# Kernel tuning notes

Measured on AMD Instinct MI355X. Metric: run time of the kernel, lower is better.

The kernel has to match this reference:

```python
import jax, jax.numpy as jnp
import numpy as np

K_GRAPH = 8
NUM_HEADS = 4


def _forward(kpt_feature, kpt_3d, gw1, gb1, gw2, gb2, w_q, b_q, w_k, b_k, w_v, b_v, w_a, b_a, w_o, b_o):
    B, N, D = kpt_feature.shape
    k = K_GRAPH
    H = NUM_HEADS
    hd = D // H

    # pairwise euclidean distances (b, N, N) -- torch.cdist equivalent
    sq = jnp.sum(kpt_3d * kpt_3d, axis=-1)
    d2 = sq[:, :, None] + sq[:, None, :] - 2.0 * jnp.einsum('bnc,bmc->bnm', kpt_3d, kpt_3d)
    dist = jnp.sqrt(jnp.maximum(d2, 0.0))

    # kNN excluding self (self-distance 0 sorts first)
    knn_idx = jnp.argsort(dist, axis=2)[:, :, 1:k + 1]  # (B, N, k)

    gather = jax.vmap(lambda arr, idx: arr[idx])  # per-batch fancy gather
    knn_pos = gather(kpt_3d, knn_idx)             # (B, N, k, 3)

    # geometry features (7-dim per edge)
    neighbor_dists = jnp.take_along_axis(dist, knn_idx, axis=2)   # (B, N, k)
    mean_dist = neighbor_dists.mean(axis=2, keepdims=True)        # (B, N, 1)
    std_dist = jnp.std(neighbor_dists, axis=2, ddof=1, keepdims=True)  # unbiased, like torch.std
    centroid = knn_pos.mean(axis=2)                               # (B, N, 3)
    rel = kpt_3d - centroid                                       # (B, N, 3)
    centered = knn_pos - centroid[:, :, None, :]                  # (B, N, k, 3)
    cov = jnp.einsum('bnkc,bnkd->bncd', centered, centered) / k   # (B, N, 3, 3)
    eig = jnp.linalg.eigvalsh(cov)                                # ascending
    aniso = eig[..., -1] / (eig[..., 0] + 1e-8)                   # (B, N)

    bcast = lambda x: jnp.broadcast_to(x[:, :, None, :], (B, N, k, x.shape[-1]))
    geom = jnp.concatenate([
        neighbor_dists[..., None],
        bcast(mean_dist),
        bcast(std_dist),
        bcast(rel),
        bcast(aniso[..., None]),
    ], axis=-1)                                                   # (B, N, k, 7)

    geom_agg = geom.mean(axis=2)                                  # (B, N, 7)
    enc = jax.nn.relu(geom_agg @ gw1.T + gb1) @ gw2.T + gb2       # (B, N, D)

    # gather-based graph attention
    knn_feat = gather(kpt_feature, knn_idx)                       # (B, N, k, D)
    Q = (kpt_feature @ w_q.T + b_q).reshape(B, N, H, hd)
    Kt = (knn_feat @ w_k.T + b_k).reshape(B, N, k, H, hd)
    Vt = (knn_feat @ w_v.T + b_v).reshape(B, N, k, H, hd)

    scores = jnp.einsum('bnhd,bnkhd->bnkh', Q, Kt) / (hd ** 0.5)  # (B, N, k, H)
    bias = geom @ w_a.T + b_a                                     # (B, N, k, H)
    attn = jax.nn.softmax(scores + bias, axis=2)
    agg = jnp.einsum('bnkh,bnkhd->bnhd', attn, Vt).reshape(B, N, D)
    graph_feat = agg @ w_o.T + b_o
    return enc + graph_feat


def setup_inputs() -> dict:
    key = jax.random.key(0)
    ks = jax.random.split(key, 20)
    B, N, D = 16, 2048, 256
    H = NUM_HEADS
    s = 0.05
    return {
        'kpt_feature': jax.random.normal(ks[0], (B, N, D), jnp.float32),
        'kpt_3d': jax.random.normal(ks[1], (B, N, 3), jnp.float32),
        'gw1': jax.random.normal(ks[2], (64, 7), jnp.float32) * s,
        'gb1': jax.random.normal(ks[3], (64,), jnp.float32) * s,
        'gw2': jax.random.normal(ks[4], (D, 64), jnp.float32) * s,
        'gb2': jax.random.normal(ks[5], (D,), jnp.float32) * s,
        'w_q': jax.random.normal(ks[6], (D, D), jnp.float32) * s,
        'b_q': jax.random.normal(ks[7], (D,), jnp.float32) * s,
        'w_k': jax.random.normal(ks[8], (D, D), jnp.float32) * s,
        'b_k': jax.random.normal(ks[9], (D,), jnp.float32) * s,
        'w_v': jax.random.normal(ks[10], (D, D), jnp.float32) * s,
        'b_v': jax.random.normal(ks[11], (D,), jnp.float32) * s,
        'w_a': jax.random.normal(ks[12], (H, 7), jnp.float32) * s,
        'b_a': jax.random.normal(ks[13], (H,), jnp.float32) * s,
        'w_o': jax.random.normal(ks[14], (D, D), jnp.float32) * s,
        'b_o': jax.random.normal(ks[15], (D,), jnp.float32) * s,
    }


def reference(kpt_feature, kpt_3d, gw1, gb1, gw2, gb2, w_q, b_q, w_k, b_k, w_v, b_v, w_a, b_a, w_o, b_o):
    return _forward(kpt_feature, kpt_3d, gw1, gb1, gw2, gb2, w_q, b_q, w_k, b_k, w_v, b_v, w_a, b_a, w_o, b_o)
```

## Files before the change

### kernel.cpp

```cpp
#include <hip/hip_runtime.h>
#include <math.h>

#define NN 2048

using f32x4 = __attribute__((ext_vector_type(4))) float;
using u32x4 = __attribute__((ext_vector_type(4))) unsigned int;
using u32x2 = __attribute__((ext_vector_type(2))) unsigned int;

__device__ __forceinline__ unsigned short f2bf(float x){
    unsigned int u = __float_as_uint(x);
    return (unsigned short)((u + 0x7FFFu + ((u>>16)&1u)) >> 16);
}
__device__ __forceinline__ float bf2f(unsigned short u){
    return __uint_as_float(((unsigned int)u) << 16);
}

__device__ __forceinline__ void mfma16(f32x4& acc, const u32x4& a, const u32x4& b) {
    asm("v_mfma_f32_16x16x32_bf16 %0, %1, %2, %0" : "+v"(acc) : "v"(a), "v"(b));
}

__device__ inline void eig3_minmax(double a11, double a12, double a13,
                                   double a22, double a23, double a33,
                                   double& lmin, double& lmax) {
    double p1 = a12*a12 + a13*a13 + a23*a23;
    double q  = (a11 + a22 + a33) / 3.0;
    double d1 = a11 - q, d2 = a22 - q, d3 = a33 - q;
    double p2 = d1*d1 + d2*d2 + d3*d3 + 2.0*p1;
    if (p2 <= 1e-300) { lmin = q; lmax = q; return; }
    double pp  = sqrt(p2 / 6.0);
    double inv = 1.0 / pp;
    double b11 = d1*inv, b22 = d2*inv, b33 = d3*inv;
    double b12 = a12*inv, b13 = a13*inv, b23 = a23*inv;
    double detB = b11*(b22*b33 - b23*b23) - b12*(b12*b33 - b23*b13) + b13*(b12*b23 - b22*b13);
    double r = detB * 0.5;
    r = fmin(1.0, fmax(-1.0, r));
    double phi = acos(r) / 3.0;
    lmax = q + 2.0*pp*cos(phi);
    lmin = q + 2.0*pp*cos(phi + 2.0943951023931953);
}

__global__ __launch_bounds__(256) void pack_pos(const float* __restrict__ k3,
                                                float4* __restrict__ pk) {
    const int i = blockIdx.x * 256 + threadIdx.x;
    const float x = k3[i*3+0], y = k3[i*3+1], z = k3[i*3+2];
    pk[i] = make_float4(x, y, z, x*x + y*y + z*z);
}

__global__ __launch_bounds__(256) void conv_feat(const float* __restrict__ in,
                                                 unsigned short* __restrict__ outb) {
    const size_t i = (size_t)(blockIdx.x * 256 + threadIdx.x) * 8;
    const float4 a = *(const float4*)(in + i);
    const float4 b = *(const float4*)(in + i + 4);
    u32x4 v;
    v.x = (unsigned)f2bf(a.x) | ((unsigned)f2bf(a.y) << 16);
    v.y = (unsigned)f2bf(a.z) | ((unsigned)f2bf(a.w) << 16);
    v.z = (unsigned)f2bf(b.x) | ((unsigned)f2bf(b.y) << 16);
    v.w = (unsigned)f2bf(b.z) | ((unsigned)f2bf(b.w) << 16);
    *(u32x4*)(outb + i) = v;
}

__global__ __launch_bounds__(256) void conv_w(
    const float* __restrict__ w_q, const float* __restrict__ w_k,
    const float* __restrict__ w_v, const float* __restrict__ w_o,
    unsigned short* __restrict__ wb) {
    const int i = blockIdx.x * 256 + threadIdx.x;
    const int sel = i >> 13;
    const size_t off = (size_t)(i & 8191) * 8;
    const float* src = (sel == 0) ? w_q : (sel == 1) ? w_k : (sel == 2) ? w_v : w_o;
    const float4 a = *(const float4*)(src + off);
    const float4 b = *(const float4*)(src + off + 4);
    u32x4 v;
    v.x = (unsigned)f2bf(a.x) | ((unsigned)f2bf(a.y) << 16);
    v.y = (unsigned)f2bf(a.z) | ((unsigned)f2bf(a.w) << 16);
    v.z = (unsigned)f2bf(b.x) | ((unsigned)f2bf(b.y) << 16);
    v.w = (unsigned)f2bf(b.z) | ((unsigned)f2bf(b.w) << 16);
    *(u32x4*)(wb + (size_t)sel * 65536 + off) = v;
}

__global__ __launch_bounds__(256) void knn_kernel(const float4* __restrict__ pk4,
                                                  int* __restrict__ idxOut) {
    __shared__ unsigned long long hitbuf[4][16];
    __shared__ int hitcnt[4];
    const int wave = threadIdx.x >> 6, lane = threadIdx.x & 63;
    const int p = blockIdx.x * 4 + wave;
    const int b = p >> 11, n = p & (NN - 1);
    const float4* pb = pk4 + (size_t)b * NN;
    const float4 me = pb[n];
    const float xn2 = -2.f*me.x, yn2 = -2.f*me.y, zn2 = -2.f*me.z, cn = me.w;

    if (lane == 0) hitcnt[wave] = 0;

    float dk[8];
    #pragma unroll
    for (int t = 0; t < 8; ++t) dk[t] = 1e30f;
    float d2s[32];

    #define INS(c4, jj, s) { \
        float d2 = cn + c4.w; \
        d2 = fmaf(xn2, c4.x, d2); \
        d2 = fmaf(yn2, c4.y, d2); \
        d2 = fmaf(zn2, c4.z, d2); \
        if ((jj) == n) d2 = 1e30f; \
        d2s[s] = d2; \
        dk[7] = __builtin_amdgcn_fmed3f(dk[6], dk[7], d2); \
        dk[6] = __builtin_amdgcn_fmed3f(dk[5], dk[6], d2); \
        dk[5] = __builtin_amdgcn_fmed3f(dk[4], dk[5], d2); \
        dk[4] = __builtin_amdgcn_fmed3f(dk[3], dk[4], d2); \
        dk[3] = __builtin_amdgcn_fmed3f(dk[2], dk[3], d2); \
        dk[2] = __builtin_amdgcn_fmed3f(dk[1], dk[2], d2); \
        dk[1] = __builtin_amdgcn_fmed3f(dk[0], dk[1], d2); \
        dk[0] = fminf(dk[0], d2); }

    #pragma unroll
    for (int i = 0; i < 8; ++i) {
        const int j0 = lane + i * 256;
        const float4 q0 = pb[j0];
        const float4 q1 = pb[j0 + 64];
        const float4 q2 = pb[j0 + 128];
        const float4 q3 = pb[j0 + 192];
        INS(q0, j0,       i*4 + 0)
        INS(q1, j0 + 64,  i*4 + 1)
        INS(q2, j0 + 128, i*4 + 2)
        INS(q3, j0 + 192, i*4 + 3)
    }
    #undef INS

    #define CSWAPV(a,c) { float lo = fminf(dk[a], dk[c]); float hi = fmaxf(dk[a], dk[c]); dk[a] = lo; dk[c] = hi; }
    #pragma unroll
    for (int m = 1; m < 64; m <<= 1) {
        float od[8];
        #pragma unroll
        for (int t = 0; t < 8; ++t) od[t] = __shfl_xor(dk[7 - t], m);
        #pragma unroll
        for (int t = 0; t < 8; ++t) dk[t] = fminf(dk[t], od[t]);
        CSWAPV(0,4) CSWAPV(1,5) CSWAPV(2,6) CSWAPV(3,7)
        CSWAPV(0,2) CSWAPV(1,3) CSWAPV(4,6) CSWAPV(5,7)
        CSWAPV(0,1) CSWAPV(2,3) CSWAPV(4,5) CSWAPV(6,7)
    }
    #undef CSWAPV

    const float tau = dk[7];

    #pragma unroll
    for (int s = 0; s < 32; ++s) {
        if (d2s[s] <= tau) {
            const int j = lane + (s >> 2) * 256 + (s & 3) * 64;
            unsigned u = __float_as_uint(d2s[s]);
            u ^= (u >> 31) ? 0xFFFFFFFFu : 0x80000000u;
            const int slot = atomicAdd(&hitcnt[wave], 1);
            if (slot < 16)
                hitbuf[wave][slot] = ((unsigned long long)u << 32) | (unsigned)j;
        }
    }

    if (lane == 0) {
        int cnt = hitcnt[wave]; if (cnt > 16) cnt = 16;
        int outv[8];
        if (cnt == 8) {
            #pragma unroll
            for (int t = 0; t < 8; ++t)
                outv[t] = (int)(unsigned)hitbuf[wave][t];
        } else {
            unsigned used = 0;
            #pragma unroll
            for (int t = 0; t < 8; ++t) {
                unsigned long long best = ~0ull; int bi = 0;
                #pragma unroll
                for (int i = 0; i < 16; ++i) {
                    unsigned long long v = (i < cnt && !((used >> i) & 1u))
                                         ? hitbuf[wave][i] : ~0ull;
                    if (v < best) { best = v; bi = i; }
                }
                used |= 1u << bi;
                outv[t] = (int)(unsigned)best;
            }
        }
        u32x4 v0; v0.x = outv[0]; v0.y = outv[1]; v0.z = outv[2]; v0.w = outv[3];
        u32x4 v1; v1.x = outv[4]; v1.y = outv[5]; v1.z = outv[6]; v1.w = outv[7];
        *(u32x4*)(idxOut + (size_t)p * 8)     = v0;
        *(u32x4*)(idxOut + (size_t)p * 8 + 4) = v1;
    }
}

__global__ __launch_bounds__(256) void geom_kernel(
    const float4* __restrict__ pk4, const int* __restrict__ knnIdx,
    const float* __restrict__ gw1, const float* __restrict__ gb1,
    const float* __restrict__ w_a, const float* __restrict__ b_a,
    float* __restrict__ biasOut, float* __restrict__ h32) {
    const int p = blockIdx.x * 256 + threadIdx.x;
    const int b = p >> 11, n = p & (NN - 1);
    const float4* pb = pk4 + (size_t)b * NN;
    const float4 me = pb[n];
    const float xn2 = -2.f*me.x, yn2 = -2.f*me.y, zn2 = -2.f*me.z, cn = me.w;

    int ik[8];
    *(u32x4*)&ik[0] = *(const u32x4*)(knnIdx + (size_t)p * 8);
    *(u32x4*)&ik[4] = *(const u32x4*)(knnIdx + (size_t)p * 8 + 4);

    float dist[8], px[8], py[8], pz[8];
    #pragma unroll
    for (int t = 0; t < 8; ++t) {
        const float4 q = pb[ik[t]];
        float d2 = cn + q.w;
        d2 = fmaf(xn2, q.x, d2);
        d2 = fmaf(yn2, q.y, d2);
        d2 = fmaf(zn2, q.z, d2);
        dist[t] = sqrtf(fmaxf(d2, 0.0f));
        px[t] = q.x; py[t] = q.y; pz[t] = q.z;
    }
    float mean = 0.f;
    #pragma unroll
    for (int t = 0; t < 8; ++t) mean += dist[t];
    mean *= 0.125f;
// ... 23 lines not shown
    float wa[28], ba[4];
    #pragma unroll
    for (int i = 0; i < 28; ++i) wa[i] = w_a[i];
    #pragma unroll
    for (int h = 0; h < 4; ++h) ba[h] = b_a[h];
    #pragma unroll
    for (int t = 0; t < 8; ++t) {
        f32x4 v;
        #pragma unroll
        for (int h = 0; h < 4; ++h) {
            v[h] = wa[h*7+0]*dist[t] + wa[h*7+1]*mean + wa[h*7+2]*stdd
                 + wa[h*7+3]*relx + wa[h*7+4]*rely + wa[h*7+5]*relz
                 + wa[h*7+6]*aniso + ba[h];
        }
        *(f32x4*)(biasOut + ((size_t)p*8 + t) * 4) = v;
    }

    const float g0 = mean, g1 = mean, g2 = stdd, g3 = relx, g4 = rely, g5 = relz, g6 = aniso;
    float* hrow = h32 + (size_t)p * 64;
    #pragma unroll
    for (int cq = 0; cq < 16; ++cq) {
        f32x4 hv;
        #pragma unroll
        for (int r = 0; r < 4; ++r) {
            const int c = cq*4 + r;
            float h = gw1[c*7+0]*g0 + gw1[c*7+1]*g1 + gw1[c*7+2]*g2 + gw1[c*7+3]*g3
                    + gw1[c*7+4]*g4 + gw1[c*7+5]*g5 + gw1[c*7+6]*g6 + gb1[c];
            hv[r] = fmaxf(h, 0.0f);
        }
        *(f32x4*)(hrow + cq*4) = hv;
    }
}

__global__ __launch_bounds__(256) void gemm_qkv_mfma(
    const unsigned short* __restrict__ Ab, const unsigned short* __restrict__ Wball,
    const float* __restrict__ b_q, const float* __restrict__ b_k, const float* __restrict__ b_v,
    float* __restrict__ Qb, unsigned short* __restrict__ Kb, unsigned short* __restrict__ Vb)
{
    __shared__ unsigned short As[128 * 72];
    __shared__ unsigned short Bs[128 * 72];
    const int tid = threadIdx.x;
    const int m0 = blockIdx.x * 128;
    const int wsel = blockIdx.y >> 1;
    const int crel0 = (blockIdx.y & 1) * 128;
    const unsigned short* Wb = Wball + (size_t)wsel * 65536;
    const float* bv = (wsel == 0) ? b_q : ((wsel == 1) ? b_k : b_v);

    const int sr = tid >> 1, sh = (tid & 1) * 32;
    const int wid = tid >> 6, lane = tid & 63;
    const int wr = (wid >> 1) * 64, wc = (wid & 1) * 64;
    const int l15 = lane & 15, lk = (lane >> 4) * 8, lq = (lane >> 4) * 4;

    f32x4 acc[4][4];
    #pragma unroll
    for (int i = 0; i < 4; ++i)
        #pragma unroll
        for (int j = 0; j < 4; ++j) { f32x4 z = {0.f,0.f,0.f,0.f}; acc[i][j] = z; }

    for (int k0 = 0; k0 < 256; k0 += 64) {
        const unsigned short* ga = Ab + (size_t)(m0 + sr) * 256 + k0 + sh;
        u32x4 a0 = *(const u32x4*)(ga);
        u32x4 a1 = *(const u32x4*)(ga + 8);
        u32x4 a2 = *(const u32x4*)(ga + 16);
        u32x4 a3 = *(const u32x4*)(ga + 24);
        const unsigned short* gw = Wb + (size_t)(crel0 + sr) * 256 + k0 + sh;
        u32x4 b0 = *(const u32x4*)(gw);
        u32x4 b1 = *(const u32x4*)(gw + 8);
        u32x4 b2 = *(const u32x4*)(gw + 16);
        u32x4 b3 = *(const u32x4*)(gw + 24);
        __syncthreads();
        *(u32x4*)&As[sr*72 + sh     ] = a0;
        *(u32x4*)&As[sr*72 + sh +  8] = a1;
        *(u32x4*)&As[sr*72 + sh + 16] = a2;
        *(u32x4*)&As[sr*72 + sh + 24] = a3;
        *(u32x4*)&Bs[sr*72 + sh     ] = b0;
        *(u32x4*)&Bs[sr*72 + sh +  8] = b1;
        *(u32x4*)&Bs[sr*72 + sh + 16] = b2;
        *(u32x4*)&Bs[sr*72 + sh + 24] = b3;
        __syncthreads();
        #pragma unroll
        for (int ks = 0; ks < 64; ks += 32) {
            u32x4 af[4], bfr[4];
            #pragma unroll
            for (int i = 0; i < 4; ++i)  af[i]  = *(const u32x4*)&As[(wr + i*16 + l15)*72 + ks + lk];
            #pragma unroll
            for (int j = 0; j < 4; ++j)  bfr[j] = *(const u32x4*)&Bs[(wc + j*16 + l15)*72 + ks + lk];
            #pragma unroll
            for (int i = 0; i < 4; ++i)
                #pragma unroll
                for (int j = 0; j < 4; ++j) mfma16(acc[i][j], af[i], bfr[j]);
        }
    }
    #pragma unroll
    for (int j = 0; j < 4; ++j) {
        const int col = crel0 + wc + j*16 + l15;
        const float biasv = bv[col];
        #pragma unroll
        for (int i = 0; i < 4; ++i)
            #pragma unroll
            for (int r = 0; r < 4; ++r) {
                const int m = m0 + wr + i*16 + lq + r;
                const float v = acc[i][j][r] + biasv;
                if (wsel == 0)      Qb[(size_t)m * 256 + col] = v;
                else if (wsel == 1) Kb[(size_t)m * 256 + col] = f2bf(v);
                else                Vb[(size_t)m * 256 + col] = f2bf(v);
            }
    }
}

__global__ __launch_bounds__(256) void gemm_o_mfma(
    const unsigned short* __restrict__ Ab, const unsigned short* __restrict__ Wb,
    const float* __restrict__ bvec, const float* addin, float* C)
{
    __shared__ unsigned short As[128 * 72];
    __shared__ unsigned short Bs[128 * 72];
    const int tid = threadIdx.x;
    const int m0 = blockIdx.x * 128;
    const int crel0 = blockIdx.y * 128;

    const int sr = tid >> 1, sh = (tid & 1) * 32;
    const int wid = tid >> 6, lane = tid & 63;
    const int wr = (wid >> 1) * 64, wc = (wid & 1) * 64;
    const int l15 = lane & 15, lk = (lane >> 4) * 8, lq = (lane >> 4) * 4;

    f32x4 acc[4][4];
    #pragma unroll
    for (int i = 0; i < 4; ++i)
        #pragma unroll
        for (int j = 0; j < 4; ++j) { f32x4 z = {0.f,0.f,0.f,0.f}; acc[i][j] = z; }

    for (int k0 = 0; k0 < 256; k0 += 64) {
        const unsigned short* ga = Ab + (size_t)(m0 + sr) * 256 + k0 + sh;
        u32x4 a0 = *(const u32x4*)(ga);
        u32x4 a1 = *(const u32x4*)(ga + 8);
        u32x4 a2 = *(const u32x4*)(ga + 16);
        u32x4 a3 = *(const u32x4*)(ga + 24);
        const unsigned short* gw = Wb + (size_t)(crel0 + sr) * 256 + k0 + sh;
        u32x4 b0 = *(const u32x4*)(gw);
        u32x4 b1 = *(const u32x4*)(gw + 8);
        u32x4 b2 = *(const u32x4*)(gw + 16);
        u32x4 b3 = *(const u32x4*)(gw + 24);
        __syncthreads();
        *(u32x4*)&As[sr*72 + sh     ] = a0;
        *(u32x4*)&As[sr*72 + sh +  8] = a1;
        *(u32x4*)&As[sr*72 + sh + 16] = a2;
        *(u32x4*)&As[sr*72 + sh + 24] = a3;
        *(u32x4*)&Bs[sr*72 + sh     ] = b0;
        *(u32x4*)&Bs[sr*72 + sh +  8] = b1;
        *(u32x4*)&Bs[sr*72 + sh + 16] = b2;
        *(u32x4*)&Bs[sr*72 + sh + 24] = b3;
        __syncthreads();
        #pragma unroll
        for (int ks = 0; ks < 64; ks += 32) {
            u32x4 af[4], bfr[4];
            #pragma unroll
            for (int i = 0; i < 4; ++i)  af[i]  = *(const u32x4*)&As[(wr + i*16 + l15)*72 + ks + lk];
            #pragma unroll
            for (int j = 0; j < 4; ++j)  bfr[j] = *(const u32x4*)&Bs[(wc + j*16 + l15)*72 + ks + lk];
            #pragma unroll
            for (int i = 0; i < 4; ++i)
                #pragma unroll
                for (int j = 0; j < 4; ++j) mfma16(acc[i][j], af[i], bfr[j]);
        }
    }
    #pragma unroll
    for (int j = 0; j < 4; ++j) {
        const int col = crel0 + wc + j*16 + l15;
        const float biasv = bvec[col];
        #pragma unroll
        for (int i = 0; i < 4; ++i)
            #pragma unroll
            for (int r = 0; r < 4; ++r) {
                const int m = m0 + wr + i*16 + lq + r;
                const float ad = addin[(size_t)m * 256 + col];
                C[(size_t)m * 256 + col] = acc[i][j][r] + biasv + ad;
            }
    }
}

template<int K>
__global__ __launch_bounds__(256) void gemm_f32_big(
    const float* __restrict__ A, const float* __restrict__ W,
    const float* __restrict__ bvec, float* __restrict__ C)
{
    __shared__ float As[16][132];
    __shared__ float Bs[16][132];
    const int tid = threadIdx.x;
    const int m0 = blockIdx.x * 128;
    const int c0 = blockIdx.y * 128;
    const int tx = tid & 15;
    const int ty = tid >> 4;
    const int lr = tid & 127;
    const int kh = (tid >> 7) * 8;

    float acc[8][8] = {};

    const float* ga = A + (size_t)(m0 + lr) * K + kh;
    const float* gb = W + (size_t)(c0 + lr) * K + kh;

    float4 av0 = *(const float4*)(ga);
    float4 av1 = *(const float4*)(ga + 4);
    float4 bv0 = *(const float4*)(gb);
    float4 bv1 = *(const float4*)(gb + 4);

    for (int k0 = 0; k0 < K; k0 += 16) {
        __syncthreads();
        As[kh+0][lr]=av0.x; As[kh+1][lr]=av0.y; As[kh+2][lr]=av0.z; As[kh+3][lr]=av0.w;
        As[kh+4][lr]=av1.x; As[kh+5][lr]=av1.y; As[kh+6][lr]=av1.z; As[kh+7][lr]=av1.w;
        Bs[kh+0][lr]=bv0.x; Bs[kh+1][lr]=bv0.y; Bs[kh+2][lr]=bv0.z; Bs[kh+3][lr]=bv0.w;
        Bs[kh+4][lr]=bv1.x; Bs[kh+5][lr]=bv1.y; Bs[kh+6][lr]=bv1.z; Bs[kh+7][lr]=bv1.w;
        if (k0 + 16 < K) {
            av0 = *(const float4*)(ga + k0 + 16);
            av1 = *(const float4*)(ga + k0 + 20);
            bv0 = *(const float4*)(gb + k0 + 16);
            bv1 = *(const float4*)(gb + k0 + 20);
        }
        __syncthreads();
        #pragma unroll
        for (int kk = 0; kk < 16; ++kk) {
            const float4 a0 = *(const float4*)&As[kk][ty*8];
            const float4 a1 = *(const float4*)&As[kk][ty*8+4];
            const float4 b0 = *(const float4*)&Bs[kk][tx*8];
            const float4 b1 = *(const float4*)&Bs[kk][tx*8+4];
            const float a[8] = {a0.x,a0.y,a0.z,a0.w,a1.x,a1.y,a1.z,a1.w};
            const float b[8] = {b0.x,b0.y,b0.z,b0.w,b1.x,b1.y,b1.z,b1.w};
            #pragma unroll
            for (int i = 0; i < 8; ++i)
                #pragma unroll
                for (int j = 0; j < 8; ++j)
                    acc[i][j] = fmaf(a[i], b[j], acc[i][j]);
        }
    }
    #pragma unroll
    for (int i = 0; i < 8; ++i) {
        const size_t m = m0 + ty*8 + i;
        const int c = c0 + tx*8;
        float4 v0, v1;
        v0.x = acc[i][0] + bvec[c+0];
        v0.y = acc[i][1] + bvec[c+1];
        v0.z = acc[i][2] + bvec[c+2];
        v0.w = acc[i][3] + bvec[c+3];
        v1.x = acc[i][4] + bvec[c+4];
        v1.y = acc[i][5] + bvec[c+5];
        v1.z = acc[i][6] + bvec[c+6];
        v1.w = acc[i][7] + bvec[c+7];
        *(float4*)(C + m*256 + c)     = v0;
        *(float4*)(C + m*256 + c + 4) = v1;
    }
}

__global__ __launch_bounds__(256) void attn_kernel(
    const float* __restrict__ Qb, const unsigned short* __restrict__ Kb,
    const unsigned short* __restrict__ Vb, const int* __restrict__ knnIdx,
    const float* __restrict__ biasb, unsigned short* __restrict__ aggb)
{
    const int wave = threadIdx.x >> 6;
    const int lane = threadIdx.x & 63;
    const int B = blockIdx.x;
    const int xcd = B & 7;
    const int k = B >> 3;
    const int batch = xcd + ((k >= 512) ? 8 : 0);
    const int p = batch * NN + ((k & 511) << 2) + wave;
    const int b = batch;
    const int h = lane >> 4;

    const float4 q = *(const float4*)(Qb + (size_t)p*256 + lane*4);

    int g[8];
    #pragma unroll
    for (int t = 0; t < 8; ++t) g[t] = b * NN + knnIdx[(size_t)p*8 + t];

    float s[8];
    #pragma unroll
    for (int t = 0; t < 8; ++t) {
        const ushort4 kv = *(const ushort4*)(Kb + (size_t)g[t]*256 + lane*4);
        float acc = q.x * bf2f(kv.x);
        acc = fmaf(q.y, bf2f(kv.y), acc);
        acc = fmaf(q.z, bf2f(kv.z), acc);
        acc = fmaf(q.w, bf2f(kv.w), acc);
        acc += __shfl_xor(acc, 1);
        acc += __shfl_xor(acc, 2);
        acc += __shfl_xor(acc, 4);
        acc += __shfl_xor(acc, 8);
        s[t] = acc * 0.125f + biasb[((size_t)p*8 + t)*4 + h];
    }

    float mx = s[0];
    #pragma unroll
    for (int t = 1; t < 8; ++t) mx = fmaxf(mx, s[t]);
    float sum = 0.f;
    #pragma unroll
    for (int t = 0; t < 8; ++t) { s[t] = expf(s[t] - mx); sum += s[t]; }
    const float inv = 1.0f / sum;

    f32x4 a = {0.f, 0.f, 0.f, 0.f};
    #pragma unroll
    for (int t = 0; t < 8; ++t) {
        const float wgt = s[t] * inv;
        const ushort4 vv = *(const ushort4*)(Vb + (size_t)g[t]*256 + lane*4);
        a[0] = fmaf(wgt, bf2f(vv.x), a[0]);
        a[1] = fmaf(wgt, bf2f(vv.y), a[1]);
        a[2] = fmaf(wgt, bf2f(vv.z), a[2]);
        a[3] = fmaf(wgt, bf2f(vv.w), a[3]);
    }
    u32x2 pk;
    pk.x = (unsigned)f2bf(a[0]) | ((unsigned)f2bf(a[1]) << 16);
    pk.y = (unsigned)f2bf(a[2]) | ((unsigned)f2bf(a[3]) << 16);
    *(u32x2*)(aggb + (size_t)p*256 + lane*4) = pk;
}

extern "C" void kernel_launch(void* const* d_in, const int* in_sizes, int n_in,
                              void* d_out, int out_size, void* d_ws, size_t ws_size,
                              hipStream_t stream) {
    const float* feat = (const float*)d_in[0];
    const float* k3   = (const float*)d_in[1];
    const float* gw1  = (const float*)d_in[2];
    const float* gb1  = (const float*)d_in[3];
    const float* gw2  = (const float*)d_in[4];
    const float* gb2  = (const float*)d_in[5];
    const float* w_q  = (const float*)d_in[6];
    const float* b_q  = (const float*)d_in[7];
    const float* w_k  = (const float*)d_in[8];
    const float* b_k  = (const float*)d_in[9];
    const float* w_v  = (const float*)d_in[10];
    const float* b_v  = (const float*)d_in[11];
    const float* w_a  = (const float*)d_in[12];
    const float* b_a  = (const float*)d_in[13];
    const float* w_o  = (const float*)d_in[14];
    const float* b_o  = (const float*)d_in[15];
    float* out = (float*)d_out;

    char* w = (char*)d_ws;
    int*            knnIdx = (int*)w;
    float*          biasb  = (float*)(w + (size_t)1*(1u<<20));
    float*          Qb     = (float*)(w + (size_t)5*(1u<<20));
    unsigned short* Kb     = (unsigned short*)(w + (size_t)37*(1u<<20));
    unsigned short* Vb     = (unsigned short*)(w + (size_t)53*(1u<<20));
    float*          h32    = (float*)(w + (size_t)69*(1u<<20));
    float4*         pk4    = (float4*)(w + (size_t)78*(1u<<20));
    unsigned short* featb  = (unsigned short*)(w + (size_t)79*(1u<<20));
    unsigned short* wb     = (unsigned short*)(w + (size_t)95*(1u<<20));
    unsigned short* aggb   = featb;

    pack_pos<<<128, 256, 0, stream>>>(k3, pk4);
    conv_feat<<<4096, 256, 0, stream>>>(feat, featb);
    conv_w<<<128, 256, 0, stream>>>(w_q, w_k, w_v, w_o, wb);
    knn_kernel<<<8192, 256, 0, stream>>>(pk4, knnIdx);
    geom_kernel<<<128, 256, 0, stream>>>(pk4, knnIdx, gw1, gb1, w_a, b_a, biasb, h32);
    gemm_f32_big<64><<<dim3(256, 2), 256, 0, stream>>>(h32, gw2, gb2, out);
    gemm_qkv_mfma<<<dim3(256, 6), 256, 0, stream>>>(featb, wb, b_q, b_k, b_v, Qb, Kb, Vb);
    attn_kernel<<<8192, 256, 0, stream>>>(Qb, Kb, Vb, knnIdx, biasb, aggb);
    gemm_o_mfma<<<dim3(256, 2), 256, 0, stream>>>(aggb, wb + (size_t)3*65536, b_o, out, out);
}
```

Measured before the change: 181.9 us.

## Merge independent kernels into block-range-dispatched fused launches

Folds the three prep kernels into one launch. kNN and the QKV GEMM, which are independent, now run in one launch whose block index selects the task, and the geometry-encoder GEMM and attention are merged the same way. This cuts launch count from nine to five and lets independent work run concurrently on the GPU to fill idle compute units. In exchange, the fused kernels carry the larger shared-memory footprint of the GEMM branch, which may lower occupancy for the kNN and attention blocks.

```diff
diff --git a/kernel.cpp b/kernel.cpp
--- a/kernel.cpp
+++ b/kernel.cpp
@@ -39,146 +39,228 @@
     lmin = q + 2.0*pp*cos(phi + 2.0943951023931953);
 }
 
-__global__ __launch_bounds__(256) void pack_pos(const float* __restrict__ k3,
-                                                float4* __restrict__ pk) {
-    const int i = blockIdx.x * 256 + threadIdx.x;
-    const float x = k3[i*3+0], y = k3[i*3+1], z = k3[i*3+2];
-    pk[i] = make_float4(x, y, z, x*x + y*y + z*z);
-}
-
-__global__ __launch_bounds__(256) void conv_feat(const float* __restrict__ in,
-                                                 unsigned short* __restrict__ outb) {
-    const size_t i = (size_t)(blockIdx.x * 256 + threadIdx.x) * 8;
-    const float4 a = *(const float4*)(in + i);
-    const float4 b = *(const float4*)(in + i + 4);
-    u32x4 v;
-    v.x = (unsigned)f2bf(a.x) | ((unsigned)f2bf(a.y) << 16);
-    v.y = (unsigned)f2bf(a.z) | ((unsigned)f2bf(a.w) << 16);
-    v.z = (unsigned)f2bf(b.x) | ((unsigned)f2bf(b.y) << 16);
-    v.w = (unsigned)f2bf(b.z) | ((unsigned)f2bf(b.w) << 16);
-    *(u32x4*)(outb + i) = v;
-}
-
-__global__ __launch_bounds__(256) void conv_w(
+__global__ __launch_bounds__(256) void prep_kernel(
+    const float* __restrict__ k3, float4* __restrict__ pk,
+    const float* __restrict__ feat, unsigned short* __restrict__ featb,
     const float* __restrict__ w_q, const float* __restrict__ w_k,
     const float* __restrict__ w_v, const float* __restrict__ w_o,
-    unsigned short* __restrict__ wb) {
-    const int i = blockIdx.x * 256 + threadIdx.x;
-    const int sel = i >> 13;
-    const size_t off = (size_t)(i & 8191) * 8;
-    const float* src = (sel == 0) ? w_q : (sel == 1) ? w_k : (sel == 2) ? w_v : w_o;
-    const float4 a = *(const float4*)(src + off);
-    const float4 b = *(const float4*)(src + off + 4);
-    u32x4 v;
-    v.x = (unsigned)f2bf(a.x) | ((unsigned)f2bf(a.y) << 16);
-    v.y = (unsigned)f2bf(a.z) | ((unsigned)f2bf(a.w) << 16);
-    v.z = (unsigned)f2bf(b.x) | ((unsigned)f2bf(b.y) << 16);
-    v.w = (unsigned)f2bf(b.z) | ((unsigned)f2bf(b.w) << 16);
-    *(u32x4*)(wb + (size_t)sel * 65536 + off) = v;
-}
-
-__global__ __launch_bounds__(256) void knn_kernel(const float4* __restrict__ pk4,
-                                                  int* __restrict__ idxOut) {
+    unsigned short* __restrict__ wb)
+{
+    const int B = blockIdx.x;
+    if (B < 128) {
+        const int i = B * 256 + threadIdx.x;
+        const float x = k3[i*3+0], y = k3[i*3+1], z = k3[i*3+2];
+        pk[i] = make_float4(x, y, z, x*x + y*y + z*z);
+    } else if (B < 4224) {
+        const size_t i = (size_t)((B - 128) * 256 + threadIdx.x) * 8;
+        const float4 a = *(const float4*)(feat + i);
+        const float4 b = *(const float4*)(feat + i + 4);
+        u32x4 v;
+        v.x = (unsigned)f2bf(a.x) | ((unsigned)f2bf(a.y) << 16);
+        v.y = (unsigned)f2bf(a.z) | ((unsigned)f2bf(a.w) << 16);
+        v.z = (unsigned)f2bf(b.x) | ((unsigned)f2bf(b.y) << 16);
+        v.w = (unsigned)f2bf(b.z) | ((unsigned)f2bf(b.w) << 16);
+        *(u32x4*)(featb + i) = v;
+    } else {
+        const int i = (B - 4224) * 256 + threadIdx.x;
+        const int sel = i >> 13;
+        const size_t off = (size_t)(i & 8191) * 8;
+        const float* src = (sel == 0) ? w_q : (sel == 1) ? w_k : (sel == 2) ? w_v : w_o;
+        const float4 a = *(const float4*)(src + off);
+        const float4 b = *(const float4*)(src + off + 4);
+        u32x4 v;
+        v.x = (unsigned)f2bf(a.x) | ((unsigned)f2bf(a.y) << 16);
+        v.y = (unsigned)f2bf(a.z) | ((unsigned)f2bf(a.w) << 16);
+        v.z = (unsigned)f2bf(b.x) | ((unsigned)f2bf(b.y) << 16);
+        v.w = (unsigned)f2bf(b.z) | ((unsigned)f2bf(b.w) << 16);
+        *(u32x4*)(wb + (size_t)sel * 65536 + off) = v;
+    }
+}
+
+__global__ __launch_bounds__(256) void fused_knn_qkv(
+    const float4* __restrict__ pk4, int* __restrict__ idxOut,
+    const unsigned short* __restrict__ Ab, const unsigned short* __restrict__ Wball,
+    const float* __restrict__ b_q, const float* __restrict__ b_k, const float* __restrict__ b_v,
+    float* __restrict__ Qb, unsigned short* __restrict__ Kb, unsigned short* __restrict__ Vb)
+{
+    __shared__ unsigned short As[128 * 72];
+    __shared__ unsigned short Bs[128 * 72];
     __shared__ unsigned long long hitbuf[4][16];
     __shared__ int hitcnt[4];
-    const int wave = threadIdx.x >> 6, lane = threadIdx.x & 63;
-    const int p = blockIdx.x * 4 + wave;
-    const int b = p >> 11, n = p & (NN - 1);
-    const float4* pb = pk4 + (size_t)b * NN;
-    const float4 me = pb[n];
-    const float xn2 = -2.f*me.x, yn2 = -2.f*me.y, zn2 = -2.f*me.z, cn = me.w;
-
-    if (lane == 0) hitcnt[wave] = 0;
-
-    float dk[8];
-    #pragma unroll
-    for (int t = 0; t < 8; ++t) dk[t] = 1e30f;
-    float d2s[32];
-
-    #define INS(c4, jj, s) { \
-        float d2 = cn + c4.w; \
-        d2 = fmaf(xn2, c4.x, d2); \
-        d2 = fmaf(yn2, c4.y, d2); \
-        d2 = fmaf(zn2, c4.z, d2); \
-        if ((jj) == n) d2 = 1e30f; \
-        d2s[s] = d2; \
-        dk[7] = __builtin_amdgcn_fmed3f(dk[6], dk[7], d2); \
-        dk[6] = __builtin_amdgcn_fmed3f(dk[5], dk[6], d2); \
-        dk[5] = __builtin_amdgcn_fmed3f(dk[4], dk[5], d2); \
-        dk[4] = __builtin_amdgcn_fmed3f(dk[3], dk[4], d2); \
-        dk[3] = __builtin_amdgcn_fmed3f(dk[2], dk[3], d2); \
-        dk[2] = __builtin_amdgcn_fmed3f(dk[1], dk[2], d2); \
-        dk[1] = __builtin_amdgcn_fmed3f(dk[0], dk[1], d2); \
-        dk[0] = fminf(dk[0], d2); }
-
-    #pragma unroll
-    for (int i = 0; i < 8; ++i) {
-        const int j0 = lane + i * 256;
-        const float4 q0 = pb[j0];
-        const float4 q1 = pb[j0 + 64];
-        const float4 q2 = pb[j0 + 128];
-        const float4 q3 = pb[j0 + 192];
-        INS(q0, j0,       i*4 + 0)
-        INS(q1, j0 + 64,  i*4 + 1)
-        INS(q2, j0 + 128, i*4 + 2)
-        INS(q3, j0 + 192, i*4 + 3)
-    }
-    #undef INS
-
-    #define CSWAPV(a,c) { float lo = fminf(dk[a], dk[c]); float hi = fmaxf(dk[a], dk[c]); dk[a] = lo; dk[c] = hi; }
-    #pragma unroll
-    for (int m = 1; m < 64; m <<= 1) {
-        float od[8];
-        #pragma unroll
-        for (int t = 0; t < 8; ++t) od[t] = __shfl_xor(dk[7 - t], m);
-        #pragma unroll
-        for (int t = 0; t < 8; ++t) dk[t] = fminf(dk[t], od[t]);
-        CSWAPV(0,4) CSWAPV(1,5) CSWAPV(2,6) CSWAPV(3,7)
-        CSWAPV(0,2) CSWAPV(1,3) CSWAPV(4,6) CSWAPV(5,7)
-        CSWAPV(0,1) CSWAPV(2,3) CSWAPV(4,5) CSWAPV(6,7)
-    }
-    #undef CSWAPV
-
-    const float tau = dk[7];
-
-    #pragma unroll
-    for (int s = 0; s < 32; ++s) {
-        if (d2s[s] <= tau) {
-            const int j = lane + (s >> 2) * 256 + (s & 3) * 64;
-            unsigned u = __float_as_uint(d2s[s]);
-            u ^= (u >> 31) ? 0xFFFFFFFFu : 0x80000000u;
-            const int slot = atomicAdd(&hitcnt[wave], 1);
-            if (slot < 16)
-                hitbuf[wave][slot] = ((unsigned long long)u << 32) | (unsigned)j;
-        }
-    }
-
-    if (lane == 0) {
-        int cnt = hitcnt[wave]; if (cnt > 16) cnt = 16;
-        int outv[8];
-        if (cnt == 8) {
-            #pragma unroll
-            for (int t = 0; t < 8; ++t)
-                outv[t] = (int)(unsigned)hitbuf[wave][t];
-        } else {
-            unsigned used = 0;
-            #pragma unroll
-            for (int t = 0; t < 8; ++t) {
-                unsigned long long best = ~0ull; int bi = 0;
-                #pragma unroll
-                for (int i = 0; i < 16; ++i) {
-                    unsigned long long v = (i < cnt && !((used >> i) & 1u))
-                                         ? hitbuf[wave][i] : ~0ull;
-                    if (v < best) { best = v; bi = i; }
+
+    const int B = blockIdx.x;
+    const int tid = threadIdx.x;
+
+    if (B < 1536) {
+        const int idx = B;
+        const int by = idx % 6;
+        const int m0 = (idx / 6) * 128;
+        const int wsel = by >> 1;
+        const int crel0 = (by & 1) * 128;
+        const unsigned short* Wb = Wball + (size_t)wsel * 65536;
+        const float* bv = (wsel == 0) ? b_q : ((wsel == 1) ? b_k : b_v);
+
+        const int sr = tid >> 1, sh = (tid & 1) * 32;
+        const int wid = tid >> 6, lane = tid & 63;
+        const int wr = (wid >> 1) * 64, wc = (wid & 1) * 64;
+        const int l15 = lane & 15, lk = (lane >> 4) * 8, lq = (lane >> 4) * 4;
+
+        f32x4 acc[4][4];
+        #pragma unroll
+        for (int i = 0; i < 4; ++i)
+            #pragma unroll
+            for (int j = 0; j < 4; ++j) { f32x4 z = {0.f,0.f,0.f,0.f}; acc[i][j] = z; }
+
+        for (int k0 = 0; k0 < 256; k0 += 64) {
+            const unsigned short* ga = Ab + (size_t)(m0 + sr) * 256 + k0 + sh;
+            u32x4 a0 = *(const u32x4*)(ga);
+            u32x4 a1 = *(const u32x4*)(ga + 8);
+            u32x4 a2 = *(const u32x4*)(ga + 16);
+            u32x4 a3 = *(const u32x4*)(ga + 24);
+            const unsigned short* gw = Wb + (size_t)(crel0 + sr) * 256 + k0 + sh;
+            u32x4 b0 = *(const u32x4*)(gw);
+            u32x4 b1 = *(const u32x4*)(gw + 8);
+            u32x4 b2 = *(const u32x4*)(gw + 16);
+            u32x4 b3 = *(const u32x4*)(gw + 24);
+            __syncthreads();
+            *(u32x4*)&As[sr*72 + sh     ] = a0;
+            *(u32x4*)&As[sr*72 + sh +  8] = a1;
+            *(u32x4*)&As[sr*72 + sh + 16] = a2;
+            *(u32x4*)&As[sr*72 + sh + 24] = a3;
+            *(u32x4*)&Bs[sr*72 + sh     ] = b0;
+            *(u32x4*)&Bs[sr*72 + sh +  8] = b1;
+            *(u32x4*)&Bs[sr*72 + sh + 16] = b2;
+            *(u32x4*)&Bs[sr*72 + sh + 24] = b3;
+            __syncthreads();
+            #pragma unroll
+            for (int ks = 0; ks < 64; ks += 32) {
+                u32x4 af[4], bfr[4];
+                #pragma unroll
+                for (int i = 0; i < 4; ++i)  af[i]  = *(const u32x4*)&As[(wr + i*16 + l15)*72 + ks + lk];
+                #pragma unroll
+                for (int j = 0; j < 4; ++j)  bfr[j] = *(const u32x4*)&Bs[(wc + j*16 + l15)*72 + ks + lk];
+                #pragma unroll
+                for (int i = 0; i < 4; ++i)
+                    #pragma unroll
+                    for (int j = 0; j < 4; ++j) mfma16(acc[i][j], af[i], bfr[j]);
+            }
+        }
+        #pragma unroll
+        for (int j = 0; j < 4; ++j) {
+            const int col = crel0 + wc + j*16 + l15;
+            const float biasv = bv[col];
+            #pragma unroll
+            for (int i = 0; i < 4; ++i)
+                #pragma unroll
+                for (int r = 0; r < 4; ++r) {
+                    const int m = m0 + wr + i*16 + lq + r;
+                    const float v = acc[i][j][r] + biasv;
+                    if (wsel == 0)      Qb[(size_t)m * 256 + col] = v;
+                    else if (wsel == 1) Kb[(size_t)m * 256 + col] = f2bf(v);
+                    else                Vb[(size_t)m * 256 + col] = f2bf(v);
                 }
-                used |= 1u << bi;
-                outv[t] = (int)(unsigned)best;
+        }
+    } else {
+        const int blk = B - 1536;
+        const int wave = tid >> 6, lane = tid & 63;
+        const int p = blk * 4 + wave;
+        const int b = p >> 11, n = p & (NN - 1);
+        const float4* pb = pk4 + (size_t)b * NN;
+        const float4 me = pb[n];
+        const float xn2 = -2.f*me.x, yn2 = -2.f*me.y, zn2 = -2.f*me.z, cn = me.w;
+
+        if (lane == 0) hitcnt[wave] = 0;
+
+        float dk[8];
+        #pragma unroll
+        for (int t = 0; t < 8; ++t) dk[t] = 1e30f;
+        float d2s[32];
+
+        #define INS(c4, jj, s) { \
+            float d2 = cn + c4.w; \
+            d2 = fmaf(xn2, c4.x, d2); \
+            d2 = fmaf(yn2, c4.y, d2); \
+            d2 = fmaf(zn2, c4.z, d2); \
+            if ((jj) == n) d2 = 1e30f; \
+            d2s[s] = d2; \
+            dk[7] = __builtin_amdgcn_fmed3f(dk[6], dk[7], d2); \
+            dk[6] = __builtin_amdgcn_fmed3f(dk[5], dk[6], d2); \
+            dk[5] = __builtin_amdgcn_fmed3f(dk[4], dk[5], d2); \
+            dk[4] = __builtin_amdgcn_fmed3f(dk[3], dk[4], d2); \
+            dk[3] = __builtin_amdgcn_fmed3f(dk[2], dk[3], d2); \
+            dk[2] = __builtin_amdgcn_fmed3f(dk[1], dk[2], d2); \
+            dk[1] = __builtin_amdgcn_fmed3f(dk[0], dk[1], d2); \
+            dk[0] = fminf(dk[0], d2); }
+
+        #pragma unroll
+        for (int i = 0; i < 8; ++i) {
+            const int j0 = lane + i * 256;
+            const float4 q0 = pb[j0];
+            const float4 q1 = pb[j0 + 64];
+            const float4 q2 = pb[j0 + 128];
+            const float4 q3 = pb[j0 + 192];
+            INS(q0, j0,       i*4 + 0)
+            INS(q1, j0 + 64,  i*4 + 1)
+            INS(q2, j0 + 128, i*4 + 2)
+            INS(q3, j0 + 192, i*4 + 3)
+        }
+        #undef INS
+
+        #define CSWAPV(a,c) { float lo = fminf(dk[a], dk[c]); float hi = fmaxf(dk[a], dk[c]); dk[a] = lo; dk[c] = hi; }
+        #pragma unroll
+        for (int m = 1; m < 64; m <<= 1) {
+            float od[8];
+            #pragma unroll
+            for (int t = 0; t < 8; ++t) od[t] = __shfl_xor(dk[7 - t], m);
+            #pragma unroll
+            for (int t = 0; t < 8; ++t) dk[t] = fminf(dk[t], od[t]);
+            CSWAPV(0,4) CSWAPV(1,5) CSWAPV(2,6) CSWAPV(3,7)
+            CSWAPV(0,2) CSWAPV(1,3) CSWAPV(4,6) CSWAPV(5,7)
+            CSWAPV(0,1) CSWAPV(2,3) CSWAPV(4,5) CSWAPV(6,7)
+        }
+        #undef CSWAPV
+
+        const float tau = dk[7];
+
+        #pragma unroll
+        for (int s = 0; s < 32; ++s) {
+            if (d2s[s] <= tau) {
+                const int j = lane + (s >> 2) * 256 + (s & 3) * 64;
+                unsigned u = __float_as_uint(d2s[s]);
+                u ^= (u >> 31) ? 0xFFFFFFFFu : 0x80000000u;
+                const int slot = atomicAdd(&hitcnt[wave], 1);
+                if (slot < 16)
+                    hitbuf[wave][slot] = ((unsigned long long)u << 32) | (unsigned)j;
             }
         }
-        u32x4 v0; v0.x = outv[0]; v0.y = outv[1]; v0.z = outv[2]; v0.w = outv[3];
-        u32x4 v1; v1.x = outv[4]; v1.y = outv[5]; v1.z = outv[6]; v1.w = outv[7];
-        *(u32x4*)(idxOut + (size_t)p * 8)     = v0;
-        *(u32x4*)(idxOut + (size_t)p * 8 + 4) = v1;
+
+        if (lane == 0) {
+            int cnt = hitcnt[wave]; if (cnt > 16) cnt = 16;
+            int outv[8];
+            if (cnt == 8) {
+                #pragma unroll
+                for (int t = 0; t < 8; ++t)
+                    outv[t] = (int)(unsigned)hitbuf[wave][t];
+            } else {
+                unsigned used = 0;
+                #pragma unroll
+                for (int t = 0; t < 8; ++t) {
+                    unsigned long long best = ~0ull; int bi = 0;
+                    #pragma unroll
+                    for (int i = 0; i < 16; ++i) {
+                        unsigned long long v = (i < cnt && !((used >> i) & 1u))
+                                             ? hitbuf[wave][i] : ~0ull;
+                        if (v < best) { best = v; bi = i; }
+                    }
+                    used |= 1u << bi;
+                    outv[t] = (int)(unsigned)best;
+                }
+            }
+            u32x4 v0; v0.x = outv[0]; v0.y = outv[1]; v0.z = outv[2]; v0.w = outv[3];
+            u32x4 v1; v1.x = outv[4]; v1.y = outv[5]; v1.z = outv[6]; v1.w = outv[7];
+            *(u32x4*)(idxOut + (size_t)p * 8)     = v0;
+            *(u32x4*)(idxOut + (size_t)p * 8 + 4) = v1;
+        }
     }
 }
 
@@ -268,19 +350,147 @@
     }
 }
 
-__global__ __launch_bounds__(256) void gemm_qkv_mfma(
-    const unsigned short* __restrict__ Ab, const unsigned short* __restrict__ Wball,
-    const float* __restrict__ b_q, const float* __restrict__ b_k, const float* __restrict__ b_v,
-    float* __restrict__ Qb, unsigned short* __restrict__ Kb, unsigned short* __restrict__ Vb)
+__global__ __launch_bounds__(256) void fused_enc_attn(
+    const float* __restrict__ h32, const float* __restrict__ gw2,
+    const float* __restrict__ gb2, float* __restrict__ encOut,
+    const float* __restrict__ Qb, const unsigned short* __restrict__ Kb,
+    const unsigned short* __restrict__ Vb, const int* __restrict__ knnIdx,
+    const float* __restrict__ biasb, unsigned short* __restrict__ aggb)
+{
+    __shared__ float As[16][132];
+    __shared__ float Bs[16][132];
+    const int Bx = blockIdx.x;
+    const int tid = threadIdx.x;
+
+    if (Bx < 512) {
+        constexpr int K = 64;
+        const int m0 = (Bx >> 1) * 128;
+        const int c0 = (Bx & 1) * 128;
+        const int tx = tid & 15;
+        const int ty = tid >> 4;
+        const int lr = tid & 127;
+        const int kh = (tid >> 7) * 8;
+
+        float acc[8][8] = {};
+
+        const float* ga = h32 + (size_t)(m0 + lr) * K + kh;
+        const float* gb = gw2 + (size_t)(c0 + lr) * K + kh;
+
+        float4 av0 = *(const float4*)(ga);
+        float4 av1 = *(const float4*)(ga + 4);
+        float4 bv0 = *(const float4*)(gb);
+        float4 bv1 = *(const float4*)(gb + 4);
+
+        for (int k0 = 0; k0 < K; k0 += 16) {
+            __syncthreads();
+            As[kh+0][lr]=av0.x; As[kh+1][lr]=av0.y; As[kh+2][lr]=av0.z; As[kh+3][lr]=av0.w;
+            As[kh+4][lr]=av1.x; As[kh+5][lr]=av1.y; As[kh+6][lr]=av1.z; As[kh+7][lr]=av1.w;
+            Bs[kh+0][lr]=bv0.x; Bs[kh+1][lr]=bv0.y; Bs[kh+2][lr]=bv0.z; Bs[kh+3][lr]=bv0.w;
+            Bs[kh+4][lr]=bv1.x; Bs[kh+5][lr]=bv1.y; Bs[kh+6][lr]=bv1.z; Bs[kh+7][lr]=bv1.w;
+            if (k0 + 16 < K) {
+                av0 = *(const float4*)(ga + k0 + 16);
+                av1 = *(const float4*)(ga + k0 + 20);
+                bv0 = *(const float4*)(gb + k0 + 16);
+                bv1 = *(const float4*)(gb + k0 + 20);
+            }
+            __syncthreads();
+            #pragma unroll
+            for (int kk = 0; kk < 16; ++kk) {
+                const float4 a0 = *(const float4*)&As[kk][ty*8];
+                const float4 a1 = *(const float4*)&As[kk][ty*8+4];
+                const float4 b0 = *(const float4*)&Bs[kk][tx*8];
+                const float4 b1 = *(const float4*)&Bs[kk][tx*8+4];
+                const float a[8] = {a0.x,a0.y,a0.z,a0.w,a1.x,a1.y,a1.z,a1.w};
+                const float b[8] = {b0.x,b0.y,b0.z,b0.w,b1.x,b1.y,b1.z,b1.w};
+                #pragma unroll
+                for (int i = 0; i < 8; ++i)
+                    #pragma unroll
+                    for (int j = 0; j < 8; ++j)
+                        acc[i][j] = fmaf(a[i], b[j], acc[i][j]);
+            }
+        }
+        #pragma unroll
+        for (int i = 0; i < 8; ++i) {
+            const size_t m = m0 + ty*8 + i;
+            const int c = c0 + tx*8;
+            float4 v0, v1;
+            v0.x = acc[i][0] + gb2[c+0];
+            v0.y = acc[i][1] + gb2[c+1];
+            v0.z = acc[i][2] + gb2[c+2];
+            v0.w = acc[i][3] + gb2[c+3];
+            v1.x = acc[i][4] + gb2[c+4];
+            v1.y = acc[i][5] + gb2[c+5];
+            v1.z = acc[i][6] + gb2[c+6];
+            v1.w = acc[i][7] + gb2[c+7];
+            *(float4*)(encOut + m*256 + c)     = v0;
+            *(float4*)(encOut + m*256 + c + 4) = v1;
+        }
+    } else {
+        const int wave = tid >> 6;
+        const int lane = tid & 63;
+        const int B = Bx - 512;
+        const int xcd = B & 7;
+        const int k = B >> 3;
+        const int batch = xcd + ((k >= 512) ? 8 : 0);
+        const int p = batch * NN + ((k & 511) << 2) + wave;
+        const int b = batch;
+        const int h = lane >> 4;
+
+        const float4 q = *(const float4*)(Qb + (size_t)p*256 + lane*4);
+
+        int g[8];
+        #pragma unroll
+        for (int t = 0; t < 8; ++t) g[t] = b * NN + knnIdx[(size_t)p*8 + t];
+
+        float s[8];
+        #pragma unroll
+        for (int t = 0; t < 8; ++t) {
+            const ushort4 kv = *(const ushort4*)(Kb + (size_t)g[t]*256 + lane*4);
+            float acc = q.x * bf2f(kv.x);
+            acc = fmaf(q.y, bf2f(kv.y), acc);
+            acc = fmaf(q.z, bf2f(kv.z), acc);
+            acc = fmaf(q.w, bf2f(kv.w), acc);
+            acc += __shfl_xor(acc, 1);
+            acc += __shfl_xor(acc, 2);
+            acc += __shfl_xor(acc, 4);
+            acc += __shfl_xor(acc, 8);
+            s[t] = acc * 0.125f + biasb[((size_t)p*8 + t)*4 + h];
+        }
+
+        float mx = s[0];
+        #pragma unroll
+        for (int t = 1; t < 8; ++t) mx = fmaxf(mx, s[t]);
+        float sum = 0.f;
+        #pragma unroll
+        for (int t = 0; t < 8; ++t) { s[t] = expf(s[t] - mx); sum += s[t]; }
+        const float inv = 1.0f / sum;
+
+        f32x4 a = {0.f, 0.f, 0.f, 0.f};
+        #pragma unroll
+        for (int t = 0; t < 8; ++t) {
+            const float wgt = s[t] * inv;
+            const ushort4 vv = *(const ushort4*)(Vb + (size_t)g[t]*256 + lane*4);
+            a[0] = fmaf(wgt, bf2f(vv.x), a[0]);
+            a[1] = fmaf(wgt, bf2f(vv.y), a[1]);
+            a[2] = fmaf(wgt, bf2f(vv.z), a[2]);
+            a[3] = fmaf(wgt, bf2f(vv.w), a[3]);
+        }
+        u32x2 pk;
+        pk.x = (unsigned)f2bf(a[0]) | ((unsigned)f2bf(a[1]) << 16);
+        pk.y = (unsigned)f2bf(a[2]) | ((unsigned)f2bf(a[3]) << 16);
+        *(u32x2*)(aggb + (size_t)p*256 + lane*4) = pk;
+    }
+}
+
+__global__ __launch_bounds__(256) void gemm_o_mfma(
+    const unsigned short* __restrict__ Ab, const unsigned short* __restrict__ Wb,
+    const float* __restrict__ bvec, const float* addin, float* C)
 {
     __shared__ unsigned short As[128 * 72];
     __shared__ unsigned short Bs[128 * 72];
     const int tid = threadIdx.x;
     const int m0 = blockIdx.x * 128;
-    const int wsel = blockIdx.y >> 1;
-    const int crel0 = (blockIdx.y & 1) * 128;
-    const unsigned short* Wb = Wball + (size_t)wsel * 65536;
-    const float* bv = (wsel == 0) ? b_q : ((wsel == 1) ? b_k : b_v);
+    const int crel0 = blockIdx.y * 128;
 
     const int sr = tid >> 1, sh = (tid & 1) * 32;
     const int wid = tid >> 6, lane = tid & 63;
@@ -330,78 +540,6 @@
     #pragma unroll
     for (int j = 0; j < 4; ++j) {
         const int col = crel0 + wc + j*16 + l15;
-        const float biasv = bv[col];
-        #pragma unroll
-        for (int i = 0; i < 4; ++i)
-            #pragma unroll
-            for (int r = 0; r < 4; ++r) {
-                const int m = m0 + wr + i*16 + lq + r;
-                const float v = acc[i][j][r] + biasv;
-                if (wsel == 0)      Qb[(size_t)m * 256 + col] = v;
-                else if (wsel == 1) Kb[(size_t)m * 256 + col] = f2bf(v);
-                else                Vb[(size_t)m * 256 + col] = f2bf(v);
-            }
-    }
-}
-
-__global__ __launch_bounds__(256) void gemm_o_mfma(
-    const unsigned short* __restrict__ Ab, const unsigned short* __restrict__ Wb,
-    const float* __restrict__ bvec, const float* addin, float* C)
-{
-    __shared__ unsigned short As[128 * 72];
-    __shared__ unsigned short Bs[128 * 72];
-    const int tid = threadIdx.x;
-    const int m0 = blockIdx.x * 128;
-    const int crel0 = blockIdx.y * 128;
-
-    const int sr = tid >> 1, sh = (tid & 1) * 32;
-    const int wid = tid >> 6, lane = tid & 63;
-    const int wr = (wid >> 1) * 64, wc = (wid & 1) * 64;
-    const int l15 = lane & 15, lk = (lane >> 4) * 8, lq = (lane >> 4) * 4;
-
-    f32x4 acc[4][4];
-    #pragma unroll
-    for (int i = 0; i < 4; ++i)
-        #pragma unroll
-        for (int j = 0; j < 4; ++j) { f32x4 z = {0.f,0.f,0.f,0.f}; acc[i][j] = z; }
-
-    for (int k0 = 0; k0 < 256; k0 += 64) {
-        const unsigned short* ga = Ab + (size_t)(m0 + sr) * 256 + k0 + sh;
-        u32x4 a0 = *(const u32x4*)(ga);
-        u32x4 a1 = *(const u32x4*)(ga + 8);
-        u32x4 a2 = *(const u32x4*)(ga + 16);
-        u32x4 a3 = *(const u32x4*)(ga + 24);
-        const unsigned short* gw = Wb + (size_t)(crel0 + sr) * 256 + k0 + sh;
-        u32x4 b0 = *(const u32x4*)(gw);
-        u32x4 b1 = *(const u32x4*)(gw + 8);
-        u32x4 b2 = *(const u32x4*)(gw + 16);
-        u32x4 b3 = *(const u32x4*)(gw + 24);
-        __syncthreads();
-        *(u32x4*)&As[sr*72 + sh     ] = a0;
-        *(u32x4*)&As[sr*72 + sh +  8] = a1;
-        *(u32x4*)&As[sr*72 + sh + 16] = a2;
-        *(u32x4*)&As[sr*72 + sh + 24] = a3;
-        *(u32x4*)&Bs[sr*72 + sh     ] = b0;
-        *(u32x4*)&Bs[sr*72 + sh +  8] = b1;
-        *(u32x4*)&Bs[sr*72 + sh + 16] = b2;
-        *(u32x4*)&Bs[sr*72 + sh + 24] = b3;
-        __syncthreads();
-        #pragma unroll
-        for (int ks = 0; ks < 64; ks += 32) {
-            u32x4 af[4], bfr[4];
-            #pragma unroll
-            for (int i = 0; i < 4; ++i)  af[i]  = *(const u32x4*)&As[(wr + i*16 + l15)*72 + ks + lk];
-            #pragma unroll
-            for (int j = 0; j < 4; ++j)  bfr[j] = *(const u32x4*)&Bs[(wc + j*16 + l15)*72 + ks + lk];
-            #pragma unroll
-            for (int i = 0; i < 4; ++i)
-                #pragma unroll
-                for (int j = 0; j < 4; ++j) mfma16(acc[i][j], af[i], bfr[j]);
-        }
-    }
-    #pragma unroll
-    for (int j = 0; j < 4; ++j) {
-        const int col = crel0 + wc + j*16 + l15;
         const float biasv = bvec[col];
         #pragma unroll
         for (int i = 0; i < 4; ++i)
@@ -412,137 +550,6 @@
                 C[(size_t)m * 256 + col] = acc[i][j][r] + biasv + ad;
             }
     }
-}
-
-template<int K>
-__global__ __launch_bounds__(256) void gemm_f32_big(
-    const float* __restrict__ A, const float* __restrict__ W,
-    const float* __restrict__ bvec, float* __restrict__ C)
-{
-    __shared__ float As[16][132];
-    __shared__ float Bs[16][132];
-    const int tid = threadIdx.x;
-    const int m0 = blockIdx.x * 128;
-    const int c0 = blockIdx.y * 128;
-    const int tx = tid & 15;
-    const int ty = tid >> 4;
-    const int lr = tid & 127;
-    const int kh = (tid >> 7) * 8;
-
-    float acc[8][8] = {};
-
-    const float* ga = A + (size_t)(m0 + lr) * K + kh;
-    const float* gb = W + (size_t)(c0 + lr) * K + kh;
-
-    float4 av0 = *(const float4*)(ga);
-    float4 av1 = *(const float4*)(ga + 4);
-    float4 bv0 = *(const float4*)(gb);
-    float4 bv1 = *(const float4*)(gb + 4);
-
-    for (int k0 = 0; k0 < K; k0 += 16) {
-        __syncthreads();
-        As[kh+0][lr]=av0.x; As[kh+1][lr]=av0.y; As[kh+2][lr]=av0.z; As[kh+3][lr]=av0.w;
-        As[kh+4][lr]=av1.x; As[kh+5][lr]=av1.y; As[kh+6][lr]=av1.z; As[kh+7][lr]=av1.w;
-        Bs[kh+0][lr]=bv0.x; Bs[kh+1][lr]=bv0.y; Bs[kh+2][lr]=bv0.z; Bs[kh+3][lr]=bv0.w;
-        Bs[kh+4][lr]=bv1.x; Bs[kh+5][lr]=bv1.y; Bs[kh+6][lr]=bv1.z; Bs[kh+7][lr]=bv1.w;
-        if (k0 + 16 < K) {
-            av0 = *(const float4*)(ga + k0 + 16);
-            av1 = *(const float4*)(ga + k0 + 20);
-            bv0 = *(const float4*)(gb + k0 + 16);
-            bv1 = *(const float4*)(gb + k0 + 20);
-        }
-        __syncthreads();
-        #pragma unroll
-        for (int kk = 0; kk < 16; ++kk) {
-            const float4 a0 = *(const float4*)&As[kk][ty*8];
-            const float4 a1 = *(const float4*)&As[kk][ty*8+4];
-            const float4 b0 = *(const float4*)&Bs[kk][tx*8];
-            const float4 b1 = *(const float4*)&Bs[kk][tx*8+4];
-            const float a[8] = {a0.x,a0.y,a0.z,a0.w,a1.x,a1.y,a1.z,a1.w};
-            const float b[8] = {b0.x,b0.y,b0.z,b0.w,b1.x,b1.y,b1.z,b1.w};
-            #pragma unroll
-            for (int i = 0; i < 8; ++i)
-                #pragma unroll
-                for (int j = 0; j < 8; ++j)
-                    acc[i][j] = fmaf(a[i], b[j], acc[i][j]);
-        }
-    }
-    #pragma unroll
-    for (int i = 0; i < 8; ++i) {
-        const size_t m = m0 + ty*8 + i;
-        const int c = c0 + tx*8;
-        float4 v0, v1;
-        v0.x = acc[i][0] + bvec[c+0];
-        v0.y = acc[i][1] + bvec[c+1];
-        v0.z = acc[i][2] + bvec[c+2];
-        v0.w = acc[i][3] + bvec[c+3];
-        v1.x = acc[i][4] + bvec[c+4];
-        v1.y = acc[i][5] + bvec[c+5];
-        v1.z = acc[i][6] + bvec[c+6];
-        v1.w = acc[i][7] + bvec[c+7];
-        *(float4*)(C + m*256 + c)     = v0;
-        *(float4*)(C + m*256 + c + 4) = v1;
-    }
-}
-
-__global__ __launch_bounds__(256) void attn_kernel(
-    const float* __restrict__ Qb, const unsigned short* __restrict__ Kb,
-    const unsigned short* __restrict__ Vb, const int* __restrict__ knnIdx,
-    const float* __restrict__ biasb, unsigned short* __restrict__ aggb)
-{
-    const int wave = threadIdx.x >> 6;
-    const int lane = threadIdx.x & 63;
-    const int B = blockIdx.x;
-    const int xcd = B & 7;
-    const int k = B >> 3;
-    const int batch = xcd + ((k >= 512) ? 8 : 0);
-    const int p = batch * NN + ((k & 511) << 2) + wave;
-    const int b = batch;
-    const int h = lane >> 4;
-
-    const float4 q = *(const float4*)(Qb + (size_t)p*256 + lane*4);
-
-    int g[8];
-    #pragma unroll
-    for (int t = 0; t < 8; ++t) g[t] = b * NN + knnIdx[(size_t)p*8 + t];
-
-    float s[8];
-    #pragma unroll
-    for (int t = 0; t < 8; ++t) {
-        const ushort4 kv = *(const ushort4*)(Kb + (size_t)g[t]*256 + lane*4);
-        float acc = q.x * bf2f(kv.x);
-        acc = fmaf(q.y, bf2f(kv.y), acc);
-        acc = fmaf(q.z, bf2f(kv.z), acc);
-        acc = fmaf(q.w, bf2f(kv.w), acc);
-        acc += __shfl_xor(acc, 1);
-        acc += __shfl_xor(acc, 2);
-        acc += __shfl_xor(acc, 4);
-        acc += __shfl_xor(acc, 8);
-        s[t] = acc * 0.125f + biasb[((size_t)p*8 + t)*4 + h];
-    }
-
-    float mx = s[0];
-    #pragma unroll
-    for (int t = 1; t < 8; ++t) mx = fmaxf(mx, s[t]);
-    float sum = 0.f;
-    #pragma unroll
-    for (int t = 0; t < 8; ++t) { s[t] = expf(s[t] - mx); sum += s[t]; }
-    const float inv = 1.0f / sum;
-
-    f32x4 a = {0.f, 0.f, 0.f, 0.f};
-    #pragma unroll
-    for (int t = 0; t < 8; ++t) {
-        const float wgt = s[t] * inv;
-        const ushort4 vv = *(const ushort4*)(Vb + (size_t)g[t]*256 + lane*4);
-        a[0] = fmaf(wgt, bf2f(vv.x), a[0]);
-        a[1] = fmaf(wgt, bf2f(vv.y), a[1]);
-        a[2] = fmaf(wgt, bf2f(vv.z), a[2]);
-        a[3] = fmaf(wgt, bf2f(vv.w), a[3]);
-    }
-    u32x2 pk;
-    pk.x = (unsigned)f2bf(a[0]) | ((unsigned)f2bf(a[1]) << 16);
-    pk.y = (unsigned)f2bf(a[2]) | ((unsigned)f2bf(a[3]) << 16);
-    *(u32x2*)(aggb + (size_t)p*256 + lane*4) = pk;
 }
 
 extern "C" void kernel_launch(void* const* d_in, const int* in_sizes, int n_in,
@@ -578,13 +585,12 @@
     unsigned short* wb     = (unsigned short*)(w + (size_t)95*(1u<<20));
     unsigned short* aggb   = featb;
 
-    pack_pos<<<128, 256, 0, stream>>>(k3, pk4);
-    conv_feat<<<4096, 256, 0, stream>>>(feat, featb);
-    conv_w<<<128, 256, 0, stream>>>(w_q, w_k, w_v, w_o, wb);
-    knn_kernel<<<8192, 256, 0, stream>>>(pk4, knnIdx);
+    prep_kernel<<<4352, 256, 0, stream>>>(k3, pk4, feat, featb,
+                                          w_q, w_k, w_v, w_o, wb);
+    fused_knn_qkv<<<9728, 256, 0, stream>>>(pk4, knnIdx, featb, wb,
+                                            b_q, b_k, b_v, Qb, Kb, Vb);
     geom_kernel<<<128, 256, 0, stream>>>(pk4, knnIdx, gw1, gb1, w_a, b_a, biasb, h32);
-    gemm_f32_big<64><<<dim3(256, 2), 256, 0, stream>>>(h32, gw2, gb2, out);
-    gemm_qkv_mfma<<<dim3(256, 6), 256, 0, stream>>>(featb, wb, b_q, b_k, b_v, Qb, Kb, Vb);
-    attn_kernel<<<8192, 256, 0, stream>>>(Qb, Kb, Vb, knnIdx, biasb, aggb);
+    fused_enc_attn<<<8704, 256, 0, stream>>>(h32, gw2, gb2, out,
+                                             Qb, Kb, Vb, knnIdx, biasb, aggb);
     gemm_o_mfma<<<dim3(256, 2), 256, 0, stream>>>(aggb, wb + (size_t)3*65536, b_o, out, out);
 }
```

Measured after the change: 190.5 us. +4.7%, slower.
